# Kernel tuning notes

Measured on AMD Instinct MI355X. Metric: run time of the kernel, lower is better.

Reference implementation:

```python
import jax, jax.numpy as jnp
import numpy as np

N_, C_, D_, H_, W_ = 2, 96, 32, 64, 64
KC, VC, HEADS = 96, 96, 4


def setup_inputs() -> dict:
    key = jax.random.key(0)
    ks = jax.random.split(key, 9)
    s = 0.05
    return {
        "x": jax.random.normal(ks[0], (N_, C_, D_, H_, W_), jnp.float32),
        "Wk": jax.random.normal(ks[1], (KC, C_), jnp.float32) * s,
        "bk": jax.random.normal(ks[2], (KC,), jnp.float32) * s,
        "Wq": jax.random.normal(ks[3], (KC, C_), jnp.float32) * s,
        "bq": jax.random.normal(ks[4], (KC,), jnp.float32) * s,
        "Wv": jax.random.normal(ks[5], (VC, C_), jnp.float32) * s,
        "bv": jax.random.normal(ks[6], (VC,), jnp.float32) * s,
        "Wr": jax.random.normal(ks[7], (C_, VC), jnp.float32) * s,
        "br": jax.random.normal(ks[8], (C_,), jnp.float32) * s,
    }


def reference(x, Wk, bk, Wq, bq, Wv, bv, Wr, br):
    n, c, d, h, w = x.shape
    Nvox = d * h * w
    xf = x.reshape(n, c, Nvox)  # [n, c, N]
    # 1x1x1 convs == channel matmuls
    keys = jnp.einsum('oc,ncN->noN', Wk, xf) + bk[None, :, None]
    queries = jnp.einsum('oc,ncN->noN', Wq, xf) + bq[None, :, None]
    values = jnp.einsum('oc,ncN->noN', Wv, xf) + bv[None, :, None]
    hk = KC // HEADS
    hv = VC // HEADS
    k = keys.reshape(n, HEADS, hk, Nvox)
    q = queries.reshape(n, HEADS, hk, Nvox)
    v = values.reshape(n, HEADS, hv, Nvox)
    # key softmax over sequence (N), query softmax over head channels (hk)
    k = jax.nn.softmax(k, axis=3)
    q = jax.nn.softmax(q, axis=2)
    # context[n,h,k,v] = key @ value^T ; attended = context^T @ query
    context = jnp.einsum('nhkN,nhvN->nhkv', k, v)
    attended = jnp.einsum('nhkv,nhkN->nhvN', context, q)
    agg = attended.reshape(n, VC, Nvox)
    out = jnp.einsum('ov,nvN->noN', Wr, agg) + br[None, :, None]
    return out.reshape(n, c, d, h, w)
```

## Files before the change

### kernel.cpp

```cpp
#include <hip/hip_runtime.h>


#define NV 131072
#define CC 96
#define NB 2
#define HK 24
#define PAD 68
#define BPN 384
#define TILES_N 2048

__global__ __launch_bounds__(256) void k_prep(
    const float* __restrict__ Wq, const float* __restrict__ Wk,
    const float* __restrict__ Wv,
    float* __restrict__ Wqt, float* __restrict__ Wkt, float* __restrict__ Wvt)
{
    const int i = blockIdx.x * 256 + threadIdx.x;
    if (i >= CC * CC) return;
    const int h = i / (HK * CC);
    const int r = i % (HK * CC);
    const int c = r / HK;
    const int j = r % HK;
    const int src = (h * HK + j) * CC + c;
    Wqt[i] = Wq[src];
    Wkt[i] = Wk[src];
    Wvt[i] = Wv[src];
}

__global__ __launch_bounds__(256) void k_fused(
    const float* __restrict__ x,
    const float* __restrict__ Wqt, const float* __restrict__ bq,
    const float* __restrict__ Wkt, const float* __restrict__ bk,
    const float* __restrict__ Wvt, const float* __restrict__ bv,
    float* __restrict__ qsm, float* __restrict__ ctx, float* __restrict__ ksum)
{
    __shared__ float eks[4 * HK * PAD];
    __shared__ float vls[4 * HK * PAD];
    const int tid = threadIdx.x;
    const int pl  = tid & 63;
    const int gu  = __builtin_amdgcn_readfirstlane(tid >> 6);
    const int n   = blockIdx.x / BPN;
    const int r0  = blockIdx.x % BPN;
    const int a   = pl >> 3, b = pl & 7;

    float* __restrict__ ek = eks + gu * HK * PAD;
    float* __restrict__ vl = vls + gu * HK * PAD;
    const float* __restrict__ Wqh = Wqt + gu * HK * CC;
    const float* __restrict__ Wkh = Wkt + gu * HK * CC;
    const float* __restrict__ Wvh = Wvt + gu * HK * CC;

    float cacc[9];
#pragma unroll
    for (int k = 0; k < 9; ++k) cacc[k] = 0.f;
    float ksacc = 0.f;

    for (int tt = r0; tt < TILES_N; tt += BPN) {
        const size_t xb = (size_t)n * CC * NV + (size_t)tt * 64 + pl;

        float aq[HK], ak[HK], av[HK];
#pragma unroll
        for (int j = 0; j < HK; ++j) {
            aq[j] = bq[gu * HK + j];
            ak[j] = bk[gu * HK + j];
            av[j] = bv[gu * HK + j];
        }
        for (int ch = 0; ch < 6; ++ch) {
            float xr[16];
#pragma unroll
            for (int u = 0; u < 16; ++u)
                xr[u] = x[xb + (size_t)(ch * 16 + u) * NV];
#pragma unroll
            for (int u = 0; u < 16; ++u) {
                const int c = ch * 16 + u;
#pragma unroll
                for (int j = 0; j < HK; ++j) {
                    aq[j] = fmaf(Wqh[c * HK + j], xr[u], aq[j]);
                    ak[j] = fmaf(Wkh[c * HK + j], xr[u], ak[j]);
                    av[j] = fmaf(Wvh[c * HK + j], xr[u], av[j]);
                }
            }
        }

        {
            float mx = aq[0];
#pragma unroll
            for (int j = 1; j < HK; ++j) mx = fmaxf(mx, aq[j]);
            float s = 0.f;
#pragma unroll
            for (int j = 0; j < HK; ++j) { aq[j] = __expf(aq[j] - mx); s += aq[j]; }
            const float inv = 1.f / s;
            const size_t qb = ((size_t)n * CC + gu * HK) * NV + (size_t)tt * 64 + pl;
#pragma unroll
            for (int j = 0; j < HK; ++j)
                qsm[qb + (size_t)j * NV] = aq[j] * inv;
        }

#pragma unroll
        for (int j = 0; j < HK; ++j) ek[j * PAD + pl] = __expf(ak[j]);
#pragma unroll
        for (int j = 0; j < HK; ++j) vl[j * PAD + pl] = av[j];

        if (pl < HK) {
            const float4* __restrict__ rp = (const float4*)(ek + pl * PAD);
            float s = 0.f;
#pragma unroll
            for (int q = 0; q < 16; ++q) {
                const float4 t = rp[q];
                s += t.x + t.y + t.z + t.w;
            }
            ksacc += s;
        }

#pragma unroll
        for (int q = 0; q < 16; ++q) {
            float4 e4[3], v4[3];
#pragma unroll
            for (int i = 0; i < 3; ++i)
                e4[i] = ((const float4*)(ek + (a + 8 * i) * PAD))[q];
#pragma unroll
            for (int j = 0; j < 3; ++j)
                v4[j] = ((const float4*)(vl + (b + 8 * j) * PAD))[q];
#pragma unroll
            for (int i = 0; i < 3; ++i)
#pragma unroll
                for (int j = 0; j < 3; ++j) {
                    float t = cacc[i * 3 + j];
                    t = fmaf(e4[i].x, v4[j].x, t);
                    t = fmaf(e4[i].y, v4[j].y, t);
                    t = fmaf(e4[i].z, v4[j].z, t);
                    t = fmaf(e4[i].w, v4[j].w, t);
                    cacc[i * 3 + j] = t;
                }
        }
    }

#pragma unroll
    for (int i = 0; i < 3; ++i)
#pragma unroll
        for (int j = 0; j < 3; ++j)
            atomicAdd(&ctx[((size_t)n * CC + gu * HK + a + 8 * i) * HK + b + 8 * j],
                      cacc[i * 3 + j]);
    if (pl < HK) atomicAdd(&ksum[n * CC + gu * HK + pl], ksacc);
}

__global__ __launch_bounds__(256) void k_combine(
    const float* __restrict__ Wr, const float* __restrict__ ctx,
    const float* __restrict__ ksum, float* __restrict__ Mnt)
{
    const int n = blockIdx.x;
    for (int i = threadIdx.x; i < CC * CC; i += 256) {
        const int kg = i / CC, o = i % CC, h = kg / HK;
        float a = 0.f;
        for (int v = 0; v < HK; ++v)
            a += Wr[o * CC + h * HK + v] * ctx[((size_t)n * CC + kg) * HK + v];
        Mnt[((size_t)n * CC + kg) * CC + o] = a / ksum[n * CC + kg];
    }
}

__global__ __launch_bounds__(256) void k_out(
    const float* __restrict__ qsm, const float* __restrict__ Mnt,
    const float* __restrict__ br, float* __restrict__ out)
{
    const int tid = threadIdx.x;
    const int pl  = tid & 63;
    const int w   = __builtin_amdgcn_readfirstlane(tid >> 6);
    const int n   = blockIdx.x >> 10;
    const int pt  = blockIdx.x & 1023;
    const size_t p0 = (size_t)pt * 128 + pl;

    const float* __restrict__ Mb = Mnt + ((size_t)n * CC) * CC + w * HK;
    const float* __restrict__ qb = qsm + (size_t)n * CC * NV + p0;

    float a0[HK], a1[HK];
#pragma unroll
    for (int j = 0; j < HK; ++j) { a0[j] = br[w * HK + j]; a1[j] = a0[j]; }

#pragma unroll 4
    for (int q = 0; q < CC; ++q) {
        const float q0 = qb[(size_t)q * NV];
        const float q1 = qb[(size_t)q * NV + 64];
        const float* __restrict__ mr = Mb + (size_t)q * CC;
#pragma unroll
        for (int j = 0; j < HK; ++j) {
            a0[j] = fmaf(mr[j], q0, a0[j]);
            a1[j] = fmaf(mr[j], q1, a1[j]);
        }
    }

    float* __restrict__ ob = out + ((size_t)n * CC + (size_t)w * HK) * NV + p0;
#pragma unroll
    for (int j = 0; j < HK; ++j) {
        ob[(size_t)j * NV]      = a0[j];
        ob[(size_t)j * NV + 64] = a1[j];
    }
}

extern "C" void kernel_launch(void* const* d_in, const int* in_sizes, int n_in,
                              void* d_out, int out_size, void* d_ws, size_t ws_size,
                              hipStream_t stream) {
    const float* x  = (const float*)d_in[0];
    const float* Wk = (const float*)d_in[1];
    const float* bk = (const float*)d_in[2];
    const float* Wq = (const float*)d_in[3];
    const float* bq = (const float*)d_in[4];
    const float* Wv = (const float*)d_in[5];
    const float* bv = (const float*)d_in[6];
    const float* Wr = (const float*)d_in[7];
    const float* br = (const float*)d_in[8];
    float* out = (float*)d_out;

    float* ws = (float*)d_ws;
    const size_t BIG = (size_t)NB * CC * NV;
    float* qsm  = ws;
    float* ctx  = ws + BIG;
    float* ksum = ctx + (size_t)NB * CC * HK;
    float* Mnt  = ksum + (size_t)NB * CC;
    float* Wqt  = Mnt + (size_t)NB * CC * CC;
    float* Wkt  = Wqt + CC * CC;
    float* Wvt  = Wkt + CC * CC;

    hipMemsetAsync(ctx, 0, ((size_t)NB * CC * HK + (size_t)NB * CC) * sizeof(float), stream);

    k_prep<<<dim3((CC * CC + 255) / 256), dim3(256), 0, stream>>>(Wq, Wk, Wv, Wqt, Wkt, Wvt);
    k_fused<<<dim3(NB * BPN), dim3(256), 0, stream>>>(x, Wqt, bq, Wkt, bk, Wvt, bv, qsm, ctx, ksum);
    k_combine<<<dim3(NB), dim3(256), 0, stream>>>(Wr, ctx, ksum, Mnt);
    k_out<<<dim3(NB * 1024), dim3(256), 0, stream>>>(qsm, Mnt, br, out);
}
```

Baseline: 572.2 us.

## Store softmaxed queries as interleaved float4 and split projection loops

The normalized query tensor is now stored with four channels packed per float4 for each voxel. The output kernel reads 16-byte vectors instead of four scalar strided loads, cutting memory transactions on the largest intermediate. The fused kernel's projection loop is also split into separate q, k and v passes over the same x registers. This may lower register pressure and change how the weight loads are scheduled.

```diff
diff --git a/kernel.cpp b/kernel.cpp
--- a/kernel.cpp
+++ b/kernel.cpp
@@ -70,13 +70,21 @@
                 xr[u] = x[xb + (size_t)(ch * 16 + u) * NV];
 #pragma unroll
             for (int u = 0; u < 16; ++u) {
-                const int c = ch * 16 + u;
-#pragma unroll
-                for (int j = 0; j < HK; ++j) {
-                    aq[j] = fmaf(Wqh[c * HK + j], xr[u], aq[j]);
-                    ak[j] = fmaf(Wkh[c * HK + j], xr[u], ak[j]);
-                    av[j] = fmaf(Wvh[c * HK + j], xr[u], av[j]);
-                }
+                const float* __restrict__ w = Wqh + (ch * 16 + u) * HK;
+#pragma unroll
+                for (int j = 0; j < HK; ++j) aq[j] = fmaf(w[j], xr[u], aq[j]);
+            }
+#pragma unroll
+            for (int u = 0; u < 16; ++u) {
+                const float* __restrict__ w = Wkh + (ch * 16 + u) * HK;
+#pragma unroll
+                for (int j = 0; j < HK; ++j) ak[j] = fmaf(w[j], xr[u], ak[j]);
+            }
+#pragma unroll
+            for (int u = 0; u < 16; ++u) {
+                const float* __restrict__ w = Wvh + (ch * 16 + u) * HK;
+#pragma unroll
+                for (int j = 0; j < HK; ++j) av[j] = fmaf(w[j], xr[u], av[j]);
             }
         }
 
@@ -88,10 +96,17 @@
 #pragma unroll
             for (int j = 0; j < HK; ++j) { aq[j] = __expf(aq[j] - mx); s += aq[j]; }
             const float inv = 1.f / s;
-            const size_t qb = ((size_t)n * CC + gu * HK) * NV + (size_t)tt * 64 + pl;
-#pragma unroll
-            for (int j = 0; j < HK; ++j)
-                qsm[qb + (size_t)j * NV] = aq[j] * inv;
+            float4* __restrict__ qs4 = (float4*)qsm;
+            const size_t qb4 = ((size_t)n * 24 + gu * 6) * NV + (size_t)tt * 64 + pl;
+#pragma unroll
+            for (int jj = 0; jj < 6; ++jj) {
+                float4 t;
+                t.x = aq[4 * jj + 0] * inv;
+                t.y = aq[4 * jj + 1] * inv;
+                t.z = aq[4 * jj + 2] * inv;
+                t.w = aq[4 * jj + 3] * inv;
+                qs4[qb4 + (size_t)jj * NV] = t;
+            }
         }
 
 #pragma unroll
@@ -168,21 +183,39 @@
     const size_t p0 = (size_t)pt * 128 + pl;
 
     const float* __restrict__ Mb = Mnt + ((size_t)n * CC) * CC + w * HK;
-    const float* __restrict__ qb = qsm + (size_t)n * CC * NV + p0;
+    const float4* __restrict__ q4 = (const float4*)qsm + (size_t)n * 24 * NV + p0;
 
     float a0[HK], a1[HK];
 #pragma unroll
     for (int j = 0; j < HK; ++j) { a0[j] = br[w * HK + j]; a1[j] = a0[j]; }
 
-#pragma unroll 4
-    for (int q = 0; q < CC; ++q) {
-        const float q0 = qb[(size_t)q * NV];
-        const float q1 = qb[(size_t)q * NV + 64];
-        const float* __restrict__ mr = Mb + (size_t)q * CC;
-#pragma unroll
-        for (int j = 0; j < HK; ++j) {
-            a0[j] = fmaf(mr[j], q0, a0[j]);
-            a1[j] = fmaf(mr[j], q1, a1[j]);
+#pragma unroll 2
+    for (int qg = 0; qg < 24; ++qg) {
+        const float4 v0 = q4[(size_t)qg * NV];
+        const float4 v1 = q4[(size_t)qg * NV + 64];
+        const float* __restrict__ m0 = Mb + (size_t)(4 * qg + 0) * CC;
+        const float* __restrict__ m1 = Mb + (size_t)(4 * qg + 1) * CC;
+        const float* __restrict__ m2 = Mb + (size_t)(4 * qg + 2) * CC;
+        const float* __restrict__ m3 = Mb + (size_t)(4 * qg + 3) * CC;
+#pragma unroll
+        for (int j = 0; j < HK; ++j) {
+            a0[j] = fmaf(m0[j], v0.x, a0[j]);
+            a1[j] = fmaf(m0[j], v1.x, a1[j]);
+        }
+#pragma unroll
+        for (int j = 0; j < HK; ++j) {
+            a0[j] = fmaf(m1[j], v0.y, a0[j]);
+            a1[j] = fmaf(m1[j], v1.y, a1[j]);
+        }
+#pragma unroll
+        for (int j = 0; j < HK; ++j) {
+            a0[j] = fmaf(m2[j], v0.z, a0[j]);
+            a1[j] = fmaf(m2[j], v1.z, a1[j]);
+        }
+#pragma unroll
+        for (int j = 0; j < HK; ++j) {
+            a0[j] = fmaf(m3[j], v0.w, a0[j]);
+            a1[j] = fmaf(m3[j], v1.w, a1[j]);
         }
     }
 
```

After: 631.8 us. 10.4% more time.
